# Performance work log

Measured on AMD Instinct MI355X. Metric: run time of the kernel, lower is better.

The kernel has to match this reference:

```python
import jax, jax.numpy as jnp
import numpy as np

N_NODES = 50000


def gcn_conv(x, W, b, edge_index, n):
    """PyG GCNConv with add_self_loops=True, normalize=True (symmetric norm)."""
    loop = jnp.arange(n, dtype=edge_index.dtype)
    row = jnp.concatenate([edge_index[0], loop])  # source
    col = jnp.concatenate([edge_index[1], loop])  # target
    ones = jnp.ones(row.shape[0], dtype=x.dtype)
    deg = jax.ops.segment_sum(ones, col, num_segments=n)
    dinv = jnp.where(deg > 0, jax.lax.rsqrt(deg), 0.0)
    norm = dinv[row] * dinv[col]  # [E+N]
    h = x @ W  # [N, hidden]
    out = jax.ops.segment_sum(h[row] * norm[:, None], col, num_segments=n)
    return out + b


def hgcn_forward(x, ei_ppi, ei_go, W0_ppi, b0_ppi, W0_go, b0_go,
                 W1_ppi, b1_ppi, W1_go, b1_go, Wc, bc, cand_edge_index):
    n = x.shape[0]
    # layer 0: HeteroConv(aggr='mean') over the two relations, then ReLU
    h = 0.5 * (gcn_conv(x, W0_ppi, b0_ppi, ei_ppi, n)
               + gcn_conv(x, W0_go, b0_go, ei_go, n))
    h = jax.nn.relu(h)
    # layer 1
    h = 0.5 * (gcn_conv(h, W1_ppi, b1_ppi, ei_ppi, n)
               + gcn_conv(h, W1_go, b1_go, ei_go, n))
    z = jax.nn.relu(h)  # [N, hidden]
    src, dst = cand_edge_index
    h_pair = jnp.concatenate([z[src], z[dst]], axis=1)  # [P, 2*hidden]
    logits = h_pair @ Wc + bc
    return z, jax.nn.sigmoid(logits)


def setup_inputs() -> dict:
    key = jax.random.key(0)
    ks = jax.random.split(key, 12)
    n, in_dim, hid, out_dim, E, P = N_NODES, 256, 128, 2, 1_000_000, 131072
    s = 1.0 / np.sqrt(in_dim)
    s2 = 1.0 / np.sqrt(hid)
    sc = 1.0 / np.sqrt(2 * hid)
    return {
        "x": jax.random.normal(ks[0], (n, in_dim), jnp.float32),
        "ei_ppi": jax.random.randint(ks[1], (2, E), 0, n, jnp.int32),
        "ei_go": jax.random.randint(ks[2], (2, E), 0, n, jnp.int32),
        "cand_edge_index": jax.random.randint(ks[3], (2, P), 0, n, jnp.int32),
        "W0_ppi": jax.random.normal(ks[4], (in_dim, hid), jnp.float32) * s,
        "b0_ppi": jnp.zeros((hid,), jnp.float32),
        "W0_go": jax.random.normal(ks[5], (in_dim, hid), jnp.float32) * s,
        "b0_go": jnp.zeros((hid,), jnp.float32),
        "W1_ppi": jax.random.normal(ks[6], (hid, hid), jnp.float32) * s2,
        "b1_ppi": jnp.zeros((hid,), jnp.float32),
        "W1_go": jax.random.normal(ks[7], (hid, hid), jnp.float32) * s2,
        "b1_go": jnp.zeros((hid,), jnp.float32),
        "Wc": jax.random.normal(ks[8], (2 * hid, out_dim), jnp.float32) * sc,
        "bc": jnp.zeros((out_dim,), jnp.float32),
    }


def reference(x, ei_ppi, ei_go, cand_edge_index, W0_ppi, b0_ppi, W0_go, b0_go,
              W1_ppi, b1_ppi, W1_go, b1_go, Wc, bc):
    return hgcn_forward(x, ei_ppi, ei_go, W0_ppi, b0_ppi, W0_go, b0_go,
                        W1_ppi, b1_ppi, W1_go, b1_go, Wc, bc, cand_edge_index)
```

## Files before the change

kernel.cpp:

```cpp
#include <hip/hip_runtime.h>
#include <math.h>

typedef _Float16 f16;
typedef f16  f16x2 __attribute__((ext_vector_type(2)));
typedef f16  f16x8 __attribute__((ext_vector_type(8)));
typedef float f32x4 __attribute__((ext_vector_type(4)));
typedef int   int4v  __attribute__((ext_vector_type(4)));

#define CAP    64
#define NBINS  125
#define SLICE  400
#define BINCAP 9216
#define ECHUNK 8192

__global__ __launch_bounds__(256) void part_kernel(
        const int* __restrict__ cols_p, const int* __restrict__ rows_p, int E1,
        const int* __restrict__ cols_g, const int* __restrict__ rows_g, int E2,
        int* __restrict__ gcur_p, int* __restrict__ gcur_g,
        unsigned* __restrict__ binbuf_p, unsigned* __restrict__ binbuf_g,
        const float* __restrict__ x, f16* __restrict__ xh, int x8,
        const float* __restrict__ W0p, const float* __restrict__ W0g,
        const float* __restrict__ W1p, const float* __restrict__ W1g,
        f16* __restrict__ T0p, f16* __restrict__ T0g,
        f16* __restrict__ T1p, f16* __restrict__ T1g,
        f16* __restrict__ zrow_p, f16* __restrict__ zrow_g,
        int EB1, int EB2, int XB) {
    const int b = blockIdx.x;
    if (b < EB1 + EB2) {
        const int sel = (b >= EB1);
        const int* cols = sel ? cols_g : cols_p;
        const int* rows = sel ? rows_g : rows_p;
        int* gcur = sel ? gcur_g : gcur_p;
        unsigned* binbuf = sel ? binbuf_g : binbuf_p;
        const int E = sel ? E2 : E1;
        const int chunk = b - (sel ? EB1 : 0);
        const int s = chunk * ECHUNK;
        const int eend = (s + ECHUNK < E) ? (s + ECHUNK) : E;
        if (s >= E) return;
        const int nE = eend - s;

        __shared__ unsigned short lc[ECHUNK];
        __shared__ int hist[NBINS], base[NBINS], cur[NBINS];
        for (int i = threadIdx.x; i < NBINS; i += 256) hist[i] = 0;
        __syncthreads();

        const int vec = nE & ~3;
        for (int i = threadIdx.x * 4; i < vec; i += 1024) {
            int4v c4 = __builtin_nontemporal_load((const int4v*)(cols + s + i));
            #pragma unroll
            for (int k = 0; k < 4; k++) {
                int c = c4[k];
                int bin = c / SLICE;
                int cl  = c - bin * SLICE;
                atomicAdd(&hist[bin], 1);
                lc[i + k] = (unsigned short)((bin << 9) | cl);
            }
        }
        for (int i = vec + threadIdx.x; i < nE; i += 256) {
            int c = cols[s + i];
            int bin = c / SLICE;
            int cl  = c - bin * SLICE;
            atomicAdd(&hist[bin], 1);
            lc[i] = (unsigned short)((bin << 9) | cl);
        }
        __syncthreads();
        if (threadIdx.x < NBINS) {
            base[threadIdx.x] = atomicAdd(&gcur[threadIdx.x], hist[threadIdx.x]);
            cur[threadIdx.x] = 0;
        }
        __syncthreads();
        for (int i = threadIdx.x; i < nE; i += 256) {
            unsigned pc = lc[i];
            int bin = pc >> 9;
            int cl  = pc & 511;
            int r   = rows[s + i];
            int p = atomicAdd(&cur[bin], 1) + base[bin];
            if (p < BINCAP)
                binbuf[(size_t)bin * BINCAP + p] = ((unsigned)r << 16) | (unsigned)cl;
        }
    } else if (b < EB1 + EB2 + XB) {
        int i = (b - EB1 - EB2) * 256 + threadIdx.x;
        if (i < x8) {
            const float4* p = (const float4*)(x + (size_t)i * 8);
            float4 a = p[0], c = p[1];
            f16x8 v = { (f16)a.x, (f16)a.y, (f16)a.z, (f16)a.w,
                        (f16)c.x, (f16)c.y, (f16)c.z, (f16)c.w };
            *(f16x8*)(xh + (size_t)i * 8) = v;
        }
    } else {
        int idx = (b - EB1 - EB2 - XB) * 256 + threadIdx.x;
        if (idx < 98304) {
            const float* W; f16* T; int K; int local;
            if (idx < 32768)      { W = W0p; T = T0p; K = 256; local = idx; }
            else if (idx < 65536) { W = W0g; T = T0g; K = 256; local = idx - 32768; }
            else if (idx < 81920) { W = W1p; T = T1p; K = 128; local = idx - 65536; }
            else                  { W = W1g; T = T1g; K = 128; local = idx - 81920; }
            int k = local >> 7, nn = local & 127;
            T[(size_t)nn * K + k] = (f16)W[local];
        } else if (idx < 98304 + 256) {
            int t = idx - 98304;
            f16x8 zv = {};
            if (t < 16)       *(f16x8*)(zrow_p + t * 8) = zv;
            else if (t < 32)  *(f16x8*)(zrow_g + (t - 16) * 8) = zv;
        }
    }
}

__global__ __launch_bounds__(256) void build_kernel(
        const unsigned* __restrict__ binbuf_p, const int* __restrict__ gcur_p,
        unsigned short* __restrict__ buf_p, int* __restrict__ cnt_p,
        const unsigned* __restrict__ binbuf_g, const int* __restrict__ gcur_g,
        unsigned short* __restrict__ buf_g, int* __restrict__ cnt_g, int n) {
    const int sel = ((int)blockIdx.x >= NBINS);
    const int bin = blockIdx.x - (sel ? NBINS : 0);
    const unsigned* binbuf = sel ? binbuf_g : binbuf_p;
    const int* gcur = sel ? gcur_g : gcur_p;
    unsigned short* buf = sel ? buf_g : buf_p;
    int* cnt = sel ? cnt_g : cnt_p;

    __shared__ unsigned short bkt[SLICE * CAP];
    __shared__ int lcnt[SLICE];
    for (int i = threadIdx.x; i < SLICE; i += 256) lcnt[i] = 0;
    __syncthreads();

    int ne = gcur[bin]; if (ne > BINCAP) ne = BINCAP;
    const unsigned* src = binbuf + (size_t)bin * BINCAP;
    for (int i = threadIdx.x; i < ne; i += 256) {
        unsigned v = src[i];
        int cl = v & 511;
        int p = atomicAdd(&lcnt[cl], 1);
        if (p < CAP) bkt[cl * CAP + p] = (unsigned short)(v >> 16);
    }
    __syncthreads();

    const int nodeBase = bin * SLICE;
    for (int i = threadIdx.x; i < SLICE; i += 256)
        if (nodeBase + i < n) cnt[nodeBase + i] = lcnt[i];
    int4v* dst = (int4v*)(buf + (size_t)nodeBase * CAP);
    const int4v* srcB = (const int4v*)bkt;
    for (int i = threadIdx.x; i < SLICE * CAP / 8; i += 256)
        dst[i] = srcB[i];
}

__global__ __launch_bounds__(256) void gemm_dual_kernel(const f16* __restrict__ A,
        const f16* __restrict__ Btp, const f16* __restrict__ Btg,
        const int* __restrict__ cnt_p, const int* __restrict__ cnt_g,
        f16* __restrict__ Cp, f16* __restrict__ Cg, int M, int K) {
    const int wave = threadIdx.x >> 6;
    const int lane = threadIdx.x & 63;
    const int m    = lane & 15;
    const int kq   = lane >> 4;
    const int row0 = blockIdx.x * 64 + wave * 16;

    int arow = row0 + m; if (arow >= M) arow = M - 1;
    const f16* ap = A + (size_t)arow * K + kq * 8;

    f32x4 accp[8], accg[8];
    #pragma unroll
    for (int t = 0; t < 8; t++) {
        accp[t] = (f32x4){0.0f, 0.0f, 0.0f, 0.0f};
        accg[t] = (f32x4){0.0f, 0.0f, 0.0f, 0.0f};
    }
    for (int k0 = 0; k0 < K; k0 += 32) {
        f16x8 a = *(const f16x8*)(ap + k0);
        #pragma unroll
        for (int t = 0; t < 8; t++) {
            f16x8 bp = *(const f16x8*)(Btp + (size_t)(t * 16 + m) * K + k0 + kq * 8);
            accp[t] = __builtin_amdgcn_mfma_f32_16x16x32_f16(a, bp, accp[t], 0, 0, 0);
            f16x8 bg = *(const f16x8*)(Btg + (size_t)(t * 16 + m) * K + k0 + kq * 8);
            accg[t] = __builtin_amdgcn_mfma_f32_16x16x32_f16(a, bg, accg[t], 0, 0, 0);
        }
    }
    #pragma unroll
    for (int r = 0; r < 4; r++) {
        int row = row0 + kq * 4 + r;
        if (row < M) {
            float sp = rsqrtf(1.0f + (float)cnt_p[row]);
            float sg = rsqrtf(1.0f + (float)cnt_g[row]);
            #pragma unroll
            for (int t = 0; t < 8; t++) {
                Cp[(size_t)row * 128 + t * 16 + m] = (f16)(accp[t][r] * sp);
                Cg[(size_t)row * 128 + t * 16 + m] = (f16)(accg[t][r] * sg);
            }
        }
    }
}

template<int OUTF32>
__global__ __launch_bounds__(256) void fused_agg_kernel(
        const f16* __restrict__ Ap, const f16* __restrict__ Ag,
        const int* __restrict__ cnt_p, const unsigned short* __restrict__ buf_p,
        const int* __restrict__ cnt_g, const unsigned short* __restrict__ buf_g,
        const float* __restrict__ b_p, const float* __restrict__ b_g,
        float* __restrict__ outf, f16* __restrict__ outh, f16* __restrict__ outh2, int n) {
    const int wave = (blockIdx.x * blockDim.x + threadIdx.x) >> 6;
    const int lane = threadIdx.x & 63;
    if (wave >= n) return;
    const int c  = wave;
    const int g  = lane >> 4;
    const int sl = lane & 15;
    const size_t fo = (size_t)sl * 8;

    float ap[8] = {}, ag[8] = {};

    {
        const unsigned short* bp = buf_p + (size_t)c * CAP;
        int deg = cnt_p[c]; if (deg > CAP) deg = CAP;
        int i = 0;
        for (; i + 8 <= deg; i += 8) {
            int r0 = bp[i + g];
            int r1 = bp[i + 4 + g];
            f16x8 v0 = *(const f16x8*)(Ap + (size_t)r0 * 128 + fo);
            f16x8 v1 = *(const f16x8*)(Ap + (size_t)r1 * 128 + fo);
            #pragma unroll
            for (int k = 0; k < 8; k++) ap[k] += (float)v0[k] + (float)v1[k];
        }
        for (; i < deg; i += 4) {
            int j = i + g;
            int r = (j < deg) ? (int)bp[j] : n;
            f16x8 v = *(const f16x8*)(Ap + (size_t)r * 128 + fo);
            #pragma unroll
            for (int k = 0; k < 8; k++) ap[k] += (float)v[k];
        }
    }
    {
        const unsigned short* bg = buf_g + (size_t)c * CAP;
        int deg = cnt_g[c]; if (deg > CAP) deg = CAP;
        int i = 0;
        for (; i + 8 <= deg; i += 8) {
            int r0 = bg[i + g];
            int r1 = bg[i + 4 + g];
            f16x8 v0 = *(const f16x8*)(Ag + (size_t)r0 * 128 + fo);
            f16x8 v1 = *(const f16x8*)(Ag + (size_t)r1 * 128 + fo);
            #pragma unroll
            for (int k = 0; k < 8; k++) ag[k] += (float)v0[k] + (float)v1[k];
        }
        for (; i < deg; i += 4) {
            int j = i + g;
            int r = (j < deg) ? (int)bg[j] : n;
            f16x8 v = *(const f16x8*)(Ag + (size_t)r * 128 + fo);
            #pragma unroll
            for (int k = 0; k < 8; k++) ag[k] += (float)v[k];
        }
    }

    #pragma unroll
    for (int k = 0; k < 8; k++) {
        ap[k] += __shfl_xor(ap[k], 16);
        ap[k] += __shfl_xor(ap[k], 32);
        ag[k] += __shfl_xor(ag[k], 16);
        ag[k] += __shfl_xor(ag[k], 32);
    }

    f16x8 selfp = *(const f16x8*)(Ap + (size_t)c * 128 + fo);
    f16x8 selfg = *(const f16x8*)(Ag + (size_t)c * 128 + fo);
    const float dpc = 0.5f * rsqrtf(1.0f + (float)cnt_p[c]);
    const float dgc = 0.5f * rsqrtf(1.0f + (float)cnt_g[c]);
    const float4* bp4 = (const float4*)(b_p + fo);
    const float4* bg4 = (const float4*)(b_g + fo);
    float4 bpa = bp4[0], bpb = bp4[1], bga = bg4[0], bgb = bg4[1];
    float bb[8] = { bpa.x + bga.x, bpa.y + bga.y, bpa.z + bga.z, bpa.w + bga.w,
                    bpb.x + bgb.x, bpb.y + bgb.y, bpb.z + bgb.z, bpb.w + bgb.w };
    float out8[8];
    #pragma unroll
    for (int k = 0; k < 8; k++) {
        float s = fmaf(dpc, ap[k] + (float)selfp[k],
                  fmaf(dgc, ag[k] + (float)selfg[k], 0.5f * bb[k]));
        out8[k] = fmaxf(s, 0.0f);
    }

    if (g == 0) {
        if (OUTF32) {
            float4 o0 = { out8[0], out8[1], out8[2], out8[3] };
            float4 o1 = { out8[4], out8[5], out8[6], out8[7] };
            float4* op = (float4*)(outf + (size_t)c * 128 + fo);
            op[0] = o0; op[1] = o1;
            f16x8 oh = { (f16)out8[0], (f16)out8[1], (f16)out8[2], (f16)out8[3],
                         (f16)out8[4], (f16)out8[5], (f16)out8[6], (f16)out8[7] };
            *(f16x8*)(outh2 + (size_t)c * 128 + fo) = oh;
        } else {
            f16x8 oh = { (f16)out8[0], (f16)out8[1], (f16)out8[2], (f16)out8[3],
                         (f16)out8[4], (f16)out8[5], (f16)out8[6], (f16)out8[7] };
            *(f16x8*)(outh + (size_t)c * 128 + fo) = oh;
        }
    }
}

__global__ __launch_bounds__(256) void pair_kernel(const f16* __restrict__ zh,
                            const int* __restrict__ src, const int* __restrict__ dst,
                            const float* __restrict__ Wc, const float* __restrict__ bc,
                            float* __restrict__ out, int P) {
    const int lane = threadIdx.x & 63;
    const int wid  = (blockIdx.x * blockDim.x + threadIdx.x) >> 6;
    const int q    = lane >> 4;
    const int sl   = lane & 15;
    const int pr   = wid * 2 + (q >> 1);
    if (pr >= P) return;
    const int node = (q & 1) ? dst[pr] : src[pr];
    f16x8 zv = *(const f16x8*)(zh + (size_t)node * 128 + sl * 8);
    const int kbase = (q & 1) * 128 + sl * 8;
    float l0 = 0.0f, l1 = 0.0f;
    #pragma unroll
    for (int k = 0; k < 8; k++) {
        float zk = (float)zv[k];
        l0 = fmaf(zk, Wc[(kbase + k) * 2 + 0], l0);
        l1 = fmaf(zk, Wc[(kbase + k) * 2 + 1], l1);
    }
    #pragma unroll
    for (int off = 1; off <= 16; off <<= 1) {
        l0 += __shfl_xor(l0, off);
        l1 += __shfl_xor(l1, off);
    }
    if ((lane & 31) == 0) {
        out[(size_t)pr * 2 + 0] = 1.0f / (1.0f + expf(-(l0 + bc[0])));
        out[(size_t)pr * 2 + 1] = 1.0f / (1.0f + expf(-(l1 + bc[1])));
    }
}

extern "C" void kernel_launch(void* const* d_in, const int* in_sizes, int n_in,
                              void* d_out, int out_size, void* d_ws, size_t ws_size,
                              hipStream_t stream) {
    const float* x      = (const float*)d_in[0];
    const int*   ei_ppi = (const int*)d_in[1];
    const int*   ei_go  = (const int*)d_in[2];
    const int*   cand   = (const int*)d_in[3];
    const float* W0_ppi = (const float*)d_in[4];
    const float* b0_ppi = (const float*)d_in[5];
    const float* W0_go  = (const float*)d_in[6];
    const float* b0_go  = (const float*)d_in[7];
    const float* W1_ppi = (const float*)d_in[8];
    const float* b1_ppi = (const float*)d_in[9];
    const float* W1_go  = (const float*)d_in[10];
    const float* b1_go  = (const float*)d_in[11];
    const float* Wc     = (const float*)d_in[12];
    const float* bc     = (const float*)d_in[13];

    const int n  = in_sizes[0] / 256;
    const int E1 = in_sizes[1] / 2;
    const int E2 = in_sizes[2] / 2;
    const int P  = in_sizes[3] / 2;

    float* z     = (float*)d_out;
    float* probs = z + (size_t)n * 128;

    const int* ppi_rows = ei_ppi;
    const int* ppi_cols = ei_ppi + E1;
    const int* go_rows  = ei_go;
    const int* go_cols  = ei_go + E2;

    const int EB1 = (E1 + ECHUNK - 1) / ECHUNK;
    const int EB2 = (E2 + ECHUNK - 1) / ECHUNK;
    const int x8 = n * 32;
    const int XB = (x8 + 255) / 256;
    const int WB = (98304 + 256 + 255) / 256;
    const int GB = (n + 63) / 64;
    const int aggGrid = (n + 3) / 4;

    size_t o = 0;
    float* ws = (float*)d_ws;
    int*   cnt_p  = (int*)(ws + o);   o += n;
    int*   cnt_g  = (int*)(ws + o);   o += n;
    int*   gcur_p = (int*)(ws + o);   o += NBINS;
    int*   gcur_g = (int*)(ws + o);   o += NBINS;
    o = (o + 3) & ~(size_t)3;
    unsigned short* buf_p = (unsigned short*)(ws + o);  o += (size_t)CAP * n / 2;
    unsigned short* buf_g = (unsigned short*)(ws + o);  o += (size_t)CAP * n / 2;
    f16*   Wt0p   = (f16*)(ws + o);   o += 256 * 128 / 2;
    f16*   Wt0g   = (f16*)(ws + o);   o += 256 * 128 / 2;
    f16*   Wt1p   = (f16*)(ws + o);   o += 128 * 128 / 2;
    f16*   Wt1g   = (f16*)(ws + o);   o += 128 * 128 / 2;
    f16*   xh     = (f16*)(ws + o);   o += (size_t)n * 256 / 2;
    f16*   A_p    = (f16*)(ws + o);   o += ((size_t)n + 1) * 128 / 2;
    f16*   A_g    = (f16*)(ws + o);   o += ((size_t)n + 1) * 128 / 2;
    f16*   h      = xh;
    f16*   zh     = xh + (size_t)n * 128;
    unsigned* binbuf_p = (unsigned*)A_p;
    unsigned* binbuf_g = binbuf_p + (size_t)NBINS * BINCAP;

    hipMemsetAsync(gcur_p, 0, (size_t)2 * NBINS * sizeof(int), stream);
    part_kernel<<<EB1 + EB2 + XB + WB, 256, 0, stream>>>(
        ppi_cols, ppi_rows, E1, go_cols, go_rows, E2,
        gcur_p, gcur_g, binbuf_p, binbuf_g,
        x, xh, x8,
        W0_ppi, W0_go, W1_ppi, W1_go, Wt0p, Wt0g, Wt1p, Wt1g,
        A_p + (size_t)n * 128, A_g + (size_t)n * 128, EB1, EB2, XB);
    build_kernel<<<2 * NBINS, 256, 0, stream>>>(
        binbuf_p, gcur_p, buf_p, cnt_p,
        binbuf_g, gcur_g, buf_g, cnt_g, n);
    gemm_dual_kernel<<<GB, 256, 0, stream>>>(xh, Wt0p, Wt0g, cnt_p, cnt_g, A_p, A_g, n, 256);
    fused_agg_kernel<0><<<aggGrid, 256, 0, stream>>>(A_p, A_g, cnt_p, buf_p,
                                                     cnt_g, buf_g,
                                                     b0_ppi, b0_go, nullptr, h, nullptr, n);
    gemm_dual_kernel<<<GB, 256, 0, stream>>>(h, Wt1p, Wt1g, cnt_p, cnt_g, A_p, A_g, n, 128);
    fused_agg_kernel<1><<<aggGrid, 256, 0, stream>>>(A_p, A_g, cnt_p, buf_p,
                                                     cnt_g, buf_g,
                                                     b1_ppi, b1_go, z, nullptr, zh, n);
    pair_kernel<<<(P + 1) / 2, 256, 0, stream>>>(zh, cand, cand + P, Wc, bc, probs, P);
}
```

Baseline: 397.9 us.

## Overlap edge partitioning with layer-0 GEMM by moving degree scaling into aggregation

The layer-0 GEMM no longer needs the degree counts, so it now runs in the same launch as the edge binning blocks, and the fp32-to-fp16 conversion moves into a separate earlier kernel. To allow this, the source-side rsqrt(deg) scaling moves out of the GEMM epilogue into the aggregation loop, where each neighbour's degree is gathered and its weight computed per edge. The workspace is reshuffled so xh aliases the bucket buffer and binbuf aliases zh, and a sentinel count slot is zeroed for the padding row. The aggregation kernel now does extra per-edge count loads and rsqrt work in exchange for removing one kernel boundary and hiding the GEMM behind partitioning.

```diff
diff --git a/kernel.cpp b/kernel.cpp
--- a/kernel.cpp
+++ b/kernel.cpp
@@ -2,7 +2,6 @@
 #include <math.h>
 
 typedef _Float16 f16;
-typedef f16  f16x2 __attribute__((ext_vector_type(2)));
 typedef f16  f16x8 __attribute__((ext_vector_type(8)));
 typedef float f32x4 __attribute__((ext_vector_type(4)));
 typedef int   int4v  __attribute__((ext_vector_type(4)));
@@ -13,73 +12,17 @@
 #define BINCAP 9216
 #define ECHUNK 8192
 
-__global__ __launch_bounds__(256) void part_kernel(
-        const int* __restrict__ cols_p, const int* __restrict__ rows_p, int E1,
-        const int* __restrict__ cols_g, const int* __restrict__ rows_g, int E2,
-        int* __restrict__ gcur_p, int* __restrict__ gcur_g,
-        unsigned* __restrict__ binbuf_p, unsigned* __restrict__ binbuf_g,
+__global__ __launch_bounds__(256) void conv_kernel(
         const float* __restrict__ x, f16* __restrict__ xh, int x8,
         const float* __restrict__ W0p, const float* __restrict__ W0g,
         const float* __restrict__ W1p, const float* __restrict__ W1g,
         f16* __restrict__ T0p, f16* __restrict__ T0g,
         f16* __restrict__ T1p, f16* __restrict__ T1g,
         f16* __restrict__ zrow_p, f16* __restrict__ zrow_g,
-        int EB1, int EB2, int XB) {
+        int* __restrict__ cnt_p, int* __restrict__ cnt_g, int n, int XB) {
     const int b = blockIdx.x;
-    if (b < EB1 + EB2) {
-        const int sel = (b >= EB1);
-        const int* cols = sel ? cols_g : cols_p;
-        const int* rows = sel ? rows_g : rows_p;
-        int* gcur = sel ? gcur_g : gcur_p;
-        unsigned* binbuf = sel ? binbuf_g : binbuf_p;
-        const int E = sel ? E2 : E1;
-        const int chunk = b - (sel ? EB1 : 0);
-        const int s = chunk * ECHUNK;
-        const int eend = (s + ECHUNK < E) ? (s + ECHUNK) : E;
-        if (s >= E) return;
-        const int nE = eend - s;
-
-        __shared__ unsigned short lc[ECHUNK];
-        __shared__ int hist[NBINS], base[NBINS], cur[NBINS];
-        for (int i = threadIdx.x; i < NBINS; i += 256) hist[i] = 0;
-        __syncthreads();
-
-        const int vec = nE & ~3;
-        for (int i = threadIdx.x * 4; i < vec; i += 1024) {
-            int4v c4 = __builtin_nontemporal_load((const int4v*)(cols + s + i));
-            #pragma unroll
-            for (int k = 0; k < 4; k++) {
-                int c = c4[k];
-                int bin = c / SLICE;
-                int cl  = c - bin * SLICE;
-                atomicAdd(&hist[bin], 1);
-                lc[i + k] = (unsigned short)((bin << 9) | cl);
-            }
-        }
-        for (int i = vec + threadIdx.x; i < nE; i += 256) {
-            int c = cols[s + i];
-            int bin = c / SLICE;
-            int cl  = c - bin * SLICE;
-            atomicAdd(&hist[bin], 1);
-            lc[i] = (unsigned short)((bin << 9) | cl);
-        }
-        __syncthreads();
-        if (threadIdx.x < NBINS) {
-            base[threadIdx.x] = atomicAdd(&gcur[threadIdx.x], hist[threadIdx.x]);
-            cur[threadIdx.x] = 0;
-        }
-        __syncthreads();
-        for (int i = threadIdx.x; i < nE; i += 256) {
-            unsigned pc = lc[i];
-            int bin = pc >> 9;
-            int cl  = pc & 511;
-            int r   = rows[s + i];
-            int p = atomicAdd(&cur[bin], 1) + base[bin];
-            if (p < BINCAP)
-                binbuf[(size_t)bin * BINCAP + p] = ((unsigned)r << 16) | (unsigned)cl;
-        }
-    } else if (b < EB1 + EB2 + XB) {
-        int i = (b - EB1 - EB2) * 256 + threadIdx.x;
+    if (b < XB) {
+        int i = b * 256 + threadIdx.x;
         if (i < x8) {
             const float4* p = (const float4*)(x + (size_t)i * 8);
             float4 a = p[0], c = p[1];
@@ -88,7 +31,7 @@
             *(f16x8*)(xh + (size_t)i * 8) = v;
         }
     } else {
-        int idx = (b - EB1 - EB2 - XB) * 256 + threadIdx.x;
+        int idx = (b - XB) * 256 + threadIdx.x;
         if (idx < 98304) {
             const float* W; f16* T; int K; int local;
             if (idx < 32768)      { W = W0p; T = T0p; K = 256; local = idx; }
@@ -102,6 +45,111 @@
             f16x8 zv = {};
             if (t < 16)       *(f16x8*)(zrow_p + t * 8) = zv;
             else if (t < 32)  *(f16x8*)(zrow_g + (t - 16) * 8) = zv;
+            else if (t == 32) cnt_p[n] = 0;
+            else if (t == 33) cnt_g[n] = 0;
+        }
+    }
+}
+
+__global__ __launch_bounds__(256) void part_gemm0_kernel(
+        const int* __restrict__ cols_p, const int* __restrict__ rows_p, int E1,
+        const int* __restrict__ cols_g, const int* __restrict__ rows_g, int E2,
+        int* __restrict__ gcur_p, int* __restrict__ gcur_g,
+        unsigned* __restrict__ binbuf_p, unsigned* __restrict__ binbuf_g,
+        int EB1, int EB2,
+        const f16* __restrict__ A, const f16* __restrict__ Btp, const f16* __restrict__ Btg,
+        f16* __restrict__ Cp, f16* __restrict__ Cg, int M, int K) {
+    const int b = blockIdx.x;
+    const int EBT = EB1 + EB2;
+    if (b < EBT) {
+        const int sel = (b >= EB1);
+        const int* cols = sel ? cols_g : cols_p;
+        const int* rows = sel ? rows_g : rows_p;
+        int* gcur = sel ? gcur_g : gcur_p;
+        unsigned* binbuf = sel ? binbuf_g : binbuf_p;
+        const int E = sel ? E2 : E1;
+        const int chunk = b - (sel ? EB1 : 0);
+        const int s = chunk * ECHUNK;
+        const int eend = (s + ECHUNK < E) ? (s + ECHUNK) : E;
+        if (s >= E) return;
+        const int nE = eend - s;
+
+        __shared__ unsigned short lc[ECHUNK];
+        __shared__ int hist[NBINS], base[NBINS], cur[NBINS];
+        for (int i = threadIdx.x; i < NBINS; i += 256) hist[i] = 0;
+        __syncthreads();
+
+        const int vec = nE & ~3;
+        for (int i = threadIdx.x * 4; i < vec; i += 1024) {
+            int4v c4 = __builtin_nontemporal_load((const int4v*)(cols + s + i));
+            #pragma unroll
+            for (int k = 0; k < 4; k++) {
+                int c = c4[k];
+                int bin = c / SLICE;
+                int cl  = c - bin * SLICE;
+                atomicAdd(&hist[bin], 1);
+                lc[i + k] = (unsigned short)((bin << 9) | cl);
+            }
+        }
+        for (int i = vec + threadIdx.x; i < nE; i += 256) {
+            int c = cols[s + i];
+            int bin = c / SLICE;
+            int cl  = c - bin * SLICE;
+            atomicAdd(&hist[bin], 1);
+            lc[i] = (unsigned short)((bin << 9) | cl);
+        }
+        __syncthreads();
+        if (threadIdx.x < NBINS) {
+            base[threadIdx.x] = atomicAdd(&gcur[threadIdx.x], hist[threadIdx.x]);
+            cur[threadIdx.x] = 0;
+        }
+        __syncthreads();
+        for (int i = threadIdx.x; i < nE; i += 256) {
+            unsigned pc = lc[i];
+            int bin = pc >> 9;
+            int cl  = pc & 511;
+            int r   = rows[s + i];
+            int p = atomicAdd(&cur[bin], 1) + base[bin];
+            if (p < BINCAP)
+                binbuf[(size_t)bin * BINCAP + p] = ((unsigned)r << 16) | (unsigned)cl;
+        }
+    } else {
+        const int bid  = b - EBT;
+        const int wave = threadIdx.x >> 6;
+        const int lane = threadIdx.x & 63;
+        const int m    = lane & 15;
+        const int kq   = lane >> 4;
+        const int row0 = bid * 64 + wave * 16;
+
+        int arow = row0 + m; if (arow >= M) arow = M - 1;
+        const f16* ap = A + (size_t)arow * K + kq * 8;
+
+        f32x4 accp[8], accg[8];
+        #pragma unroll
+        for (int t = 0; t < 8; t++) {
+            accp[t] = (f32x4){0.0f, 0.0f, 0.0f, 0.0f};
+            accg[t] = (f32x4){0.0f, 0.0f, 0.0f, 0.0f};
+        }
+        for (int k0 = 0; k0 < K; k0 += 32) {
+            f16x8 a = *(const f16x8*)(ap + k0);
+            #pragma unroll
+            for (int t = 0; t < 8; t++) {
+                f16x8 bp = *(const f16x8*)(Btp + (size_t)(t * 16 + m) * K + k0 + kq * 8);
+                accp[t] = __builtin_amdgcn_mfma_f32_16x16x32_f16(a, bp, accp[t], 0, 0, 0);
+                f16x8 bg = *(const f16x8*)(Btg + (size_t)(t * 16 + m) * K + k0 + kq * 8);
+                accg[t] = __builtin_amdgcn_mfma_f32_16x16x32_f16(a, bg, accg[t], 0, 0, 0);
+            }
+        }
+        #pragma unroll
+        for (int r = 0; r < 4; r++) {
+            int row = row0 + kq * 4 + r;
+            if (row < M) {
+                #pragma unroll
+                for (int t = 0; t < 8; t++) {
+                    Cp[(size_t)row * 128 + t * 16 + m] = (f16)accp[t][r];
+                    Cg[(size_t)row * 128 + t * 16 + m] = (f16)accg[t][r];
+                }
+            }
         }
     }
 }
@@ -144,7 +192,6 @@
 
 __global__ __launch_bounds__(256) void gemm_dual_kernel(const f16* __restrict__ A,
         const f16* __restrict__ Btp, const f16* __restrict__ Btg,
-        const int* __restrict__ cnt_p, const int* __restrict__ cnt_g,
         f16* __restrict__ Cp, f16* __restrict__ Cg, int M, int K) {
     const int wave = threadIdx.x >> 6;
     const int lane = threadIdx.x & 63;
@@ -175,12 +222,10 @@
     for (int r = 0; r < 4; r++) {
         int row = row0 + kq * 4 + r;
         if (row < M) {
-            float sp = rsqrtf(1.0f + (float)cnt_p[row]);
-            float sg = rsqrtf(1.0f + (float)cnt_g[row]);
             #pragma unroll
             for (int t = 0; t < 8; t++) {
-                Cp[(size_t)row * 128 + t * 16 + m] = (f16)(accp[t][r] * sp);
-                Cg[(size_t)row * 128 + t * 16 + m] = (f16)(accg[t][r] * sg);
+                Cp[(size_t)row * 128 + t * 16 + m] = (f16)accp[t][r];
+                Cg[(size_t)row * 128 + t * 16 + m] = (f16)accg[t][r];
             }
         }
     }
@@ -201,61 +246,78 @@
     const int sl = lane & 15;
     const size_t fo = (size_t)sl * 8;
 
-    float ap[8] = {}, ag[8] = {};
+    const int degp_t = cnt_p[c];
+    const int degg_t = cnt_g[c];
+    const int degp = (degp_t > CAP) ? CAP : degp_t;
+    const int degg = (degg_t > CAP) ? CAP : degg_t;
+    const float dvpc = rsqrtf(1.0f + (float)degp_t);
+    const float dvgc = rsqrtf(1.0f + (float)degg_t);
+    const float dpc = 0.5f * dvpc;
+    const float dgc = 0.5f * dvgc;
+    const unsigned short* bp = buf_p + (size_t)c * CAP;
+    const unsigned short* bg = buf_g + (size_t)c * CAP;
+
+    float acc[8] = {};
 
     {
-        const unsigned short* bp = buf_p + (size_t)c * CAP;
-        int deg = cnt_p[c]; if (deg > CAP) deg = CAP;
         int i = 0;
-        for (; i + 8 <= deg; i += 8) {
+        for (; i + 8 <= degp; i += 8) {
             int r0 = bp[i + g];
             int r1 = bp[i + 4 + g];
+            float w0 = dpc * rsqrtf(1.0f + (float)cnt_p[r0]);
+            float w1 = dpc * rsqrtf(1.0f + (float)cnt_p[r1]);
             f16x8 v0 = *(const f16x8*)(Ap + (size_t)r0 * 128 + fo);
             f16x8 v1 = *(const f16x8*)(Ap + (size_t)r1 * 128 + fo);
             #pragma unroll
-            for (int k = 0; k < 8; k++) ap[k] += (float)v0[k] + (float)v1[k];
-        }
-        for (; i < deg; i += 4) {
+            for (int k = 0; k < 8; k++) {
+                acc[k] = fmaf(w0, (float)v0[k], acc[k]);
+                acc[k] = fmaf(w1, (float)v1[k], acc[k]);
+            }
+        }
+        for (; i < degp; i += 4) {
             int j = i + g;
-            int r = (j < deg) ? (int)bp[j] : n;
+            int r = (j < degp) ? (int)bp[j] : n;
+            float w = dpc * rsqrtf(1.0f + (float)cnt_p[r]);
             f16x8 v = *(const f16x8*)(Ap + (size_t)r * 128 + fo);
             #pragma unroll
-            for (int k = 0; k < 8; k++) ap[k] += (float)v[k];
+            for (int k = 0; k < 8; k++) acc[k] = fmaf(w, (float)v[k], acc[k]);
         }
     }
     {
-        const unsigned short* bg = buf_g + (size_t)c * CAP;
-        int deg = cnt_g[c]; if (deg > CAP) deg = CAP;
         int i = 0;
-        for (; i + 8 <= deg; i += 8) {
+        for (; i + 8 <= degg; i += 8) {
             int r0 = bg[i + g];
             int r1 = bg[i + 4 + g];
+            float w0 = dgc * rsqrtf(1.0f + (float)cnt_g[r0]);
+            float w1 = dgc * rsqrtf(1.0f + (float)cnt_g[r1]);
             f16x8 v0 = *(const f16x8*)(Ag + (size_t)r0 * 128 + fo);
             f16x8 v1 = *(const f16x8*)(Ag + (size_t)r1 * 128 + fo);
             #pragma unroll
-            for (int k = 0; k < 8; k++) ag[k] += (float)v0[k] + (float)v1[k];
-        }
-        for (; i < deg; i += 4) {
+            for (int k = 0; k < 8; k++) {
+                acc[k] = fmaf(w0, (float)v0[k], acc[k]);
+                acc[k] = fmaf(w1, (float)v1[k], acc[k]);
+            }
+        }
+        for (; i < degg; i += 4) {
             int j = i + g;
-            int r = (j < deg) ? (int)bg[j] : n;
+            int r = (j < degg) ? (int)bg[j] : n;
+            float w = dgc * rsqrtf(1.0f + (float)cnt_g[r]);
             f16x8 v = *(const f16x8*)(Ag + (size_t)r * 128 + fo);
             #pragma unroll
-            for (int k = 0; k < 8; k++) ag[k] += (float)v[k];
+            for (int k = 0; k < 8; k++) acc[k] = fmaf(w, (float)v[k], acc[k]);
         }
     }
 
     #pragma unroll
     for (int k = 0; k < 8; k++) {
-        ap[k] += __shfl_xor(ap[k], 16);
-        ap[k] += __shfl_xor(ap[k], 32);
-        ag[k] += __shfl_xor(ag[k], 16);
-        ag[k] += __shfl_xor(ag[k], 32);
+        acc[k] += __shfl_xor(acc[k], 16);
+        acc[k] += __shfl_xor(acc[k], 32);
     }
 
     f16x8 selfp = *(const f16x8*)(Ap + (size_t)c * 128 + fo);
     f16x8 selfg = *(const f16x8*)(Ag + (size_t)c * 128 + fo);
-    const float dpc = 0.5f * rsqrtf(1.0f + (float)cnt_p[c]);
-    const float dgc = 0.5f * rsqrtf(1.0f + (float)cnt_g[c]);
+    const float swp = dpc * dvpc;
+    const float swg = dgc * dvgc;
     const float4* bp4 = (const float4*)(b_p + fo);
     const float4* bg4 = (const float4*)(b_g + fo);
     float4 bpa = bp4[0], bpb = bp4[1], bga = bg4[0], bgb = bg4[1];
@@ -264,8 +326,7 @@
     float out8[8];
     #pragma unroll
     for (int k = 0; k < 8; k++) {
-        float s = fmaf(dpc, ap[k] + (float)selfp[k],
-                  fmaf(dgc, ag[k] + (float)selfg[k], 0.5f * bb[k]));
+        float s = acc[k] + swp * (float)selfp[k] + swg * (float)selfg[k] + 0.5f * bb[k];
         out8[k] = fmaxf(s, 0.0f);
     }
 
@@ -358,40 +419,40 @@
 
     size_t o = 0;
     float* ws = (float*)d_ws;
-    int*   cnt_p  = (int*)(ws + o);   o += n;
-    int*   cnt_g  = (int*)(ws + o);   o += n;
+    int*   cnt_p  = (int*)(ws + o);   o += n + 1;
+    int*   cnt_g  = (int*)(ws + o);   o += n + 1;
     int*   gcur_p = (int*)(ws + o);   o += NBINS;
     int*   gcur_g = (int*)(ws + o);   o += NBINS;
     o = (o + 3) & ~(size_t)3;
     unsigned short* buf_p = (unsigned short*)(ws + o);  o += (size_t)CAP * n / 2;
     unsigned short* buf_g = (unsigned short*)(ws + o);  o += (size_t)CAP * n / 2;
+    f16*   h      = (f16*)(ws + o);   o += (size_t)n * 128 / 2;
+    f16*   zh     = (f16*)(ws + o);   o += (size_t)n * 128 / 2;
     f16*   Wt0p   = (f16*)(ws + o);   o += 256 * 128 / 2;
     f16*   Wt0g   = (f16*)(ws + o);   o += 256 * 128 / 2;
     f16*   Wt1p   = (f16*)(ws + o);   o += 128 * 128 / 2;
     f16*   Wt1g   = (f16*)(ws + o);   o += 128 * 128 / 2;
-    f16*   xh     = (f16*)(ws + o);   o += (size_t)n * 256 / 2;
     f16*   A_p    = (f16*)(ws + o);   o += ((size_t)n + 1) * 128 / 2;
     f16*   A_g    = (f16*)(ws + o);   o += ((size_t)n + 1) * 128 / 2;
-    f16*   h      = xh;
-    f16*   zh     = xh + (size_t)n * 128;
-    unsigned* binbuf_p = (unsigned*)A_p;
+    f16*      xh       = (f16*)buf_p;
+    unsigned* binbuf_p = (unsigned*)zh;
     unsigned* binbuf_g = binbuf_p + (size_t)NBINS * BINCAP;
 
     hipMemsetAsync(gcur_p, 0, (size_t)2 * NBINS * sizeof(int), stream);
-    part_kernel<<<EB1 + EB2 + XB + WB, 256, 0, stream>>>(
+    conv_kernel<<<XB + WB, 256, 0, stream>>>(
+        x, xh, x8, W0_ppi, W0_go, W1_ppi, W1_go, Wt0p, Wt0g, Wt1p, Wt1g,
+        A_p + (size_t)n * 128, A_g + (size_t)n * 128, cnt_p, cnt_g, n, XB);
+    part_gemm0_kernel<<<EB1 + EB2 + GB, 256, 0, stream>>>(
         ppi_cols, ppi_rows, E1, go_cols, go_rows, E2,
-        gcur_p, gcur_g, binbuf_p, binbuf_g,
-        x, xh, x8,
-        W0_ppi, W0_go, W1_ppi, W1_go, Wt0p, Wt0g, Wt1p, Wt1g,
-        A_p + (size_t)n * 128, A_g + (size_t)n * 128, EB1, EB2, XB);
+        gcur_p, gcur_g, binbuf_p, binbuf_g, EB1, EB2,
+        xh, Wt0p, Wt0g, A_p, A_g, n, 256);
     build_kernel<<<2 * NBINS, 256, 0, stream>>>(
         binbuf_p, gcur_p, buf_p, cnt_p,
         binbuf_g, gcur_g, buf_g, cnt_g, n);
-    gemm_dual_kernel<<<GB, 256, 0, stream>>>(xh, Wt0p, Wt0g, cnt_p, cnt_g, A_p, A_g, n, 256);
     fused_agg_kernel<0><<<aggGrid, 256, 0, stream>>>(A_p, A_g, cnt_p, buf_p,
                                                      cnt_g, buf_g,
                                                      b0_ppi, b0_go, nullptr, h, nullptr, n);
-    gemm_dual_kernel<<<GB, 256, 0, stream>>>(h, Wt1p, Wt1g, cnt_p, cnt_g, A_p, A_g, n, 128);
+    gemm_dual_kernel<<<GB, 256, 0, stream>>>(h, Wt1p, Wt1g, A_p, A_g, n, 128);
     fused_agg_kernel<1><<<aggGrid, 256, 0, stream>>>(A_p, A_g, cnt_p, buf_p,
                                                      cnt_g, buf_g,
                                                      b1_ppi, b1_go, z, nullptr, zh, n);
```

After: 386.4 us. -2.9%, faster.
